# Optimization experiments

Hardware: AMD Instinct MI355X
Metric: run time of the kernel (lower is better)

## Reference

```python
import jax, jax.numpy as jnp
import numpy as np

N_NODES = 50000
N_EDGES = 400000
NUM_FEAT = 11
HID = 64
LAT = 64
HEADS = 3
MAX_NODES = 29
NUM_GRAPHS = 2048
NEG_SLOPE = 0.2


def _w(key, shape):
    return (jax.random.normal(key, shape) * 0.05).astype(jnp.float32)


def setup_inputs() -> dict:
    key = jax.random.key(0)
    ks = jax.random.split(key, 32)
    x = jax.random.normal(ks[0], (N_NODES, NUM_FEAT), dtype=jnp.float32)
    edge_index = jax.random.randint(ks[1], (2, N_EDGES), 0, N_NODES, dtype=jnp.int64)
    batch = jnp.sort(jax.random.randint(ks[2], (N_NODES,), 0, NUM_GRAPHS, dtype=jnp.int64))
    d = {"x": x, "edge_index": edge_index, "batch": batch}
    # GATv2 layer params: lin_l, lin_r ([in, heads*out]), att [heads,out], bias [out]
    dims = [(NUM_FEAT, HID), (HID, 2 * HID), (2 * HID, 4 * HID)]
    k = 3
    for i, (cin, cout) in enumerate(dims, start=1):
        d[f"Wl{i}"] = _w(ks[k], (cin, HEADS * cout)); k += 1
        d[f"bl{i}"] = jnp.zeros((HEADS * cout,), jnp.float32)
        d[f"Wr{i}"] = _w(ks[k], (cin, HEADS * cout)); k += 1
        d[f"br{i}"] = jnp.zeros((HEADS * cout,), jnp.float32)
        d[f"att{i}"] = _w(ks[k], (HEADS, cout)); k += 1
        d[f"b{i}"] = jnp.zeros((cout,), jnp.float32)
    d["Wmu"] = _w(ks[k], (4 * HID, LAT)); k += 1
    d["bmu"] = jnp.zeros((LAT,), jnp.float32)
    d["Wlv"] = _w(ks[k], (4 * HID, LAT)); k += 1
    d["blv"] = jnp.zeros((LAT,), jnp.float32)
    out_dim = MAX_NODES * NUM_FEAT + MAX_NODES * MAX_NODES
    d["Wd1"] = _w(ks[k], (LAT, 4 * HID)); k += 1
    d["bd1"] = jnp.zeros((4 * HID,), jnp.float32)
    d["Wd2"] = _w(ks[k], (4 * HID, 8 * HID)); k += 1
    d["bd2"] = jnp.zeros((8 * HID,), jnp.float32)
    d["Wd3"] = _w(ks[k], (8 * HID, out_dim)); k += 1
    d["bd3"] = jnp.zeros((out_dim,), jnp.float32)
    return d


def _gatv2(x, src, dst, Wl, bl, Wr, br, att, bias):
    # GATv2Conv, heads=HEADS, concat=False (mean over heads), self-loops already in src/dst
    N = x.shape[0]
    H, C = att.shape
    xl = (x @ Wl + bl).reshape(N, H, C)  # source transform
    xr = (x @ Wr + br).reshape(N, H, C)  # target transform
    e = jax.nn.leaky_relu(xl[src] + xr[dst], NEG_SLOPE)  # [E,H,C]
    logits = jnp.einsum('ehc,hc->eh', e, att)            # [E,H]
    mx = jax.ops.segment_max(logits, dst, num_segments=N)
    a = jnp.exp(logits - mx[dst])
    denom = jax.ops.segment_sum(a, dst, num_segments=N)
    alpha = a / (denom[dst] + 1e-16)
    out = jax.ops.segment_sum(alpha[:, :, None] * xl[src], dst, num_segments=N)  # [N,H,C]
    return out.mean(axis=1) + bias


def reference(x, edge_index, batch,
              Wl1, bl1, Wr1, br1, att1, b1,
              Wl2, bl2, Wr2, br2, att2, b2,
              Wl3, bl3, Wr3, br3, att3, b3,
              Wmu, bmu, Wlv, blv,
              Wd1, bd1, Wd2, bd2, Wd3, bd3):
    N = x.shape[0]
    loops = jnp.arange(N, dtype=edge_index.dtype)
    src = jnp.concatenate([edge_index[0], loops])
    dst = jnp.concatenate([edge_index[1], loops])
    h = jax.nn.relu(_gatv2(x, src, dst, Wl1, bl1, Wr1, br1, att1, b1))
    h = jax.nn.relu(_gatv2(h, src, dst, Wl2, bl2, Wr2, br2, att2, b2))
    h = jax.nn.relu(_gatv2(h, src, dst, Wl3, bl3, Wr3, br3, att3, b3))
    g = jax.ops.segment_sum(h, batch, num_segments=NUM_GRAPHS)  # global_add_pool
    mu = g @ Wmu + bmu
    logvar = g @ Wlv + blv
    z = mu  # deterministic decode of the posterior mean (no forward() given)
    o = jax.nn.relu(z @ Wd1 + bd1)
    o = jax.nn.relu(o @ Wd2 + bd2)
    o = o @ Wd3 + bd3
    nsplit = MAX_NODES * NUM_FEAT
    x_rec = o[:, :nsplit].reshape(-1, MAX_NODES, NUM_FEAT)
    adj = o[:, nsplit:].reshape(-1, MAX_NODES, MAX_NODES)
    adj_rec = (adj + jnp.swapaxes(adj, 1, 2)) / 2
    return (x_rec, adj_rec, mu, logvar)
```

## Files before the change

### kernel.cpp

```cpp
#include <hip/hip_runtime.h>
#include <hip/hip_bf16.h>

typedef __hip_bfloat16 bf16;
typedef unsigned short ushortT;
typedef ushortT u16x1 __attribute__((ext_vector_type(1)));
typedef ushortT u16x2 __attribute__((ext_vector_type(2)));
typedef ushortT u16x4 __attribute__((ext_vector_type(4)));
typedef ushortT u16x8 __attribute__((ext_vector_type(8)));
typedef __bf16   bf16x8 __attribute__((ext_vector_type(8)));
typedef float    f32x4  __attribute__((ext_vector_type(4)));

#define N_NODES    50000
#define E_EDGES    400000
#define E_TOT      450000
#define NUM_GRAPHS 2048
#define SCAN_CHUNK 1024
#define N_CHUNKS   ((N_NODES + SCAN_CHUNK - 1) / SCAN_CHUNK)

__device__ __forceinline__ float fromb(ushortT u) {
    unsigned int i = ((unsigned int)u) << 16;
    return __builtin_bit_cast(float, i);
}
__device__ __forceinline__ ushortT tob(float v) {
    bf16 h = __float2bfloat16(v);
    return __builtin_bit_cast(ushortT, h);
}

template <int VEC> struct RawV;
template <> struct RawV<1> { using T = u16x1; };
template <> struct RawV<2> { using T = u16x2; };
template <> struct RawV<4> { using T = u16x4; };

__device__ __forceinline__ void cvtv(u16x1 r, float* f) { f[0] = fromb(r[0]); }
__device__ __forceinline__ void cvtv(u16x2 r, float* f) { f[0] = fromb(r.x); f[1] = fromb(r.y); }
__device__ __forceinline__ void cvtv(u16x4 r, float* f) { f[0] = fromb(r.x); f[1] = fromb(r.y);
                                                          f[2] = fromb(r.z); f[3] = fromb(r.w); }

__global__ void diag_kernel(float* out, float v) { if (threadIdx.x == 0) out[0] = v; }

__global__ void hist_kernel(const int* __restrict__ ei, int* __restrict__ counts) {
    int e = blockIdx.x * 256 + threadIdx.x;
    if (e >= E_TOT) return;
    int d = (e < E_EDGES) ? ei[E_EDGES + e] : (e - E_EDGES);
    atomicAdd(&counts[d], 1);
}

__global__ __launch_bounds__(256) void scan_sums(const int* __restrict__ counts,
                                                 int* __restrict__ chunk_sums) {
    __shared__ int red[4];
    int base = blockIdx.x * SCAN_CHUNK;
    int t = threadIdx.x;
    int s = 0;
    #pragma unroll
    for (int i = 0; i < 4; i++) {
        int idx = base + t + i * 256;
        if (idx < N_NODES) s += counts[idx];
    }
    #pragma unroll
    for (int o = 32; o > 0; o >>= 1) s += __shfl_xor(s, o);
    if ((t & 63) == 0) red[t >> 6] = s;
    __syncthreads();
    if (t == 0) chunk_sums[blockIdx.x] = red[0] + red[1] + red[2] + red[3];
}

__global__ __launch_bounds__(64) void scan_chunks(const int* __restrict__ chunk_sums,
                                                  int* __restrict__ chunk_base) {
    int t = threadIdx.x;
    int v = (t < N_CHUNKS) ? chunk_sums[t] : 0;
    int orig = v;
    #pragma unroll
    for (int o = 1; o < 64; o <<= 1) {
        int u = __shfl_up(v, o);
        if (t >= o) v += u;
    }
    if (t < N_CHUNKS) chunk_base[t] = v - orig;
}

__global__ __launch_bounds__(256) void scan_write(const int* __restrict__ counts,
                                                  const int* __restrict__ chunk_base,
                                                  int* __restrict__ offsets,
                                                  int* __restrict__ cursor) {
    __shared__ int wsum[4];
    int chunk = blockIdx.x;
    int base = chunk * SCAN_CHUNK;
    int t = threadIdx.x;
    int lane = t & 63, w = t >> 6;

    int c[4];
    int e0 = base + t * 4;
    #pragma unroll
    for (int k = 0; k < 4; k++) {
        int idx = e0 + k;
        c[k] = (idx < N_NODES) ? counts[idx] : 0;
    }
    int local = c[0] + c[1] + c[2] + c[3];

    int v = local;
    #pragma unroll
    for (int o = 1; o < 64; o <<= 1) {
        int u = __shfl_up(v, o);
        if (lane >= o) v += u;
    }
    if (lane == 63) wsum[w] = v;
    __syncthreads();
    int wbase = 0;
    for (int i = 0; i < w; i++) wbase += wsum[i];

    int run = chunk_base[chunk] + wbase + (v - local);
    #pragma unroll
    for (int k = 0; k < 4; k++) {
        int idx = e0 + k;
        if (idx < N_NODES) { offsets[idx] = run; cursor[idx] = run; }
        run += c[k];
    }
    if (chunk == 0 && t == 0) offsets[N_NODES] = E_TOT;
}

__global__ void scatter_kernel(const int* __restrict__ ei, int* __restrict__ cursor,
                               int* __restrict__ srcs) {
    int e = blockIdx.x * 256 + threadIdx.x;
    if (e >= E_TOT) return;
    int s, d;
    if (e < E_EDGES) { s = ei[e]; d = ei[E_EDGES + e]; }
    else             { s = d = e - E_EDGES; }
    int pos = atomicAdd(&cursor[d], 1);
    srcs[pos] = s;
}

__global__ void repack_gat_kernel(const float* __restrict__ Wl2, const float* __restrict__ Wr2,
                                  const float* __restrict__ Wl3, const float* __restrict__ Wr3,
                                  ushortT* __restrict__ BpL2, ushortT* __restrict__ BpR2,
                                  ushortT* __restrict__ BpL3, ushortT* __restrict__ BpR3) {
    const int S2 = 64 * 384, S3 = 128 * 768;
    int idx = blockIdx.x * 256 + threadIdx.x;
    const float* W; ushortT* Bp; int N, local;
    if (idx < S2)                { W = Wl2; Bp = BpL2; N = 384; local = idx; }
    else if (idx < 2 * S2)       { W = Wr2; Bp = BpR2; N = 384; local = idx - S2; }
    else if (idx < 2 * S2 + S3)  { W = Wl3; Bp = BpL3; N = 768; local = idx - 2 * S2; }
    else if (idx < 2 * (S2 + S3)){ W = Wr3; Bp = BpR3; N = 768; local = idx - 2 * S2 - S3; }
    else return;
    int k = local / N, n = local % N;
    Bp[((size_t)(k >> 3) * N + n) * 8 + (k & 7)] = tob(W[(size_t)k * N + n]);
}

__global__ void repack_split3(const float* __restrict__ Wd1, const float* __restrict__ Wd2,
                              const float* __restrict__ Wd3,
                              ushortT* __restrict__ BhD1, ushortT* __restrict__ BlD1,
                              ushortT* __restrict__ BhD2, ushortT* __restrict__ BlD2,
                              ushortT* __restrict__ BhD3, ushortT* __restrict__ BlD3) {
    const int T1 = 64 * 256, T2 = 256 * 512, T3 = 512 * 1280;
    int idx = blockIdx.x * 256 + threadIdx.x;
    const float* W; ushortT *Bh, *Bl; int Npad, N, local;
    if (idx < T1)                { W = Wd1; Bh = BhD1; Bl = BlD1; Npad = 256;  N = 256;  local = idx; }
    else if (idx < T1 + T2)      { W = Wd2; Bh = BhD2; Bl = BlD2; Npad = 512;  N = 512;  local = idx - T1; }
    else if (idx < T1 + T2 + T3) { W = Wd3; Bh = BhD3; Bl = BlD3; Npad = 1280; N = 1160; local = idx - T1 - T2; }
    else return;
    int k = local / Npad, n = local % Npad;
    float v = (n < N) ? W[(size_t)k * N + n] : 0.f;
    ushortT h = tob(v);
    size_t o = ((size_t)(k >> 3) * Npad + n) * 8 + (k & 7);
    Bh[o] = h;
    Bl[o] = tob(v - fromb(h));
}

__global__ __launch_bounds__(192) void l1_transform(const float* __restrict__ x,
                                                    const float* __restrict__ Wl,
                                                    const float* __restrict__ bl,
                                                    const float* __restrict__ Wr,
                                                    const float* __restrict__ br,
                                                    ushortT* __restrict__ XL,
                                                    ushortT* __restrict__ XR, int M) {
    __shared__ float xs[64][11];
    const int tid = threadIdx.x;
    const int bm  = blockIdx.x * 64;
    const int rows = (M - bm < 64) ? (M - bm) : 64;

    float wl[11], wr[11];
    #pragma unroll
    for (int k = 0; k < 11; k++) {
        wl[k] = Wl[k * 192 + tid];
        wr[k] = Wr[k * 192 + tid];
    }
    float blc = bl[tid], brc = br[tid];

    for (int i = tid; i < rows * 11; i += 192)
        xs[i / 11][i % 11] = x[(size_t)bm * 11 + i];
    __syncthreads();

    for (int r = 0; r < rows; r++) {
        float al = blc, ar = brc;
        #pragma unroll
        for (int k = 0; k < 11; k++) {
            float xv = xs[r][k];
            al += xv * wl[k];
            ar += xv * wr[k];
        }
        size_t o = (size_t)(bm + r) * 192 + tid;
        XL[o] = tob(al);
        XR[o] = tob(ar);
    }
}

template <bool RELU>
__global__ __launch_bounds__(256) void gemm_dec(const float* __restrict__ A,
                                                const float* __restrict__ B,
                                                const float* __restrict__ bias,
                                                float* __restrict__ C,
                                                int M, int N, int K,
                                                int lda, int ldb, int ldc) {
    __shared__ float As[32][33];
    __shared__ float Bs[32][65];
    int tid = threadIdx.x;
    int tm = tid >> 4, tn = tid & 15;
    int bm = blockIdx.y * 32, bn = blockIdx.x * 64;
    float acc[2][4] = {};
    for (int k0 = 0; k0 < K; k0 += 32) {
        #pragma unroll
        for (int i = 0; i < 4; i++) {
            int e = tid + i * 256;
            int r = e >> 5, k = e & 31;
            int row = bm + r, kk = k0 + k;
            float v = 0.f;
            if (row < M && kk < K) v = A[(size_t)row * lda + kk];
            As[k][r] = v;
        }
        #pragma unroll
        for (int i = 0; i < 8; i++) {
            int e = tid + i * 256;
            int k = e >> 6, n = e & 63;
            int kk = k0 + k, col = bn + n;
            float v = 0.f;
            if (kk < K && col < N) v = B[(size_t)kk * ldb + col];
            Bs[k][n] = v;
        }
        __syncthreads();
        #pragma unroll
        for (int k = 0; k < 32; k++) {
            float a0 = As[k][tm * 2 + 0], a1 = As[k][tm * 2 + 1];
            float b0 = Bs[k][tn * 4 + 0], b1 = Bs[k][tn * 4 + 1];
            float b2 = Bs[k][tn * 4 + 2], b3 = Bs[k][tn * 4 + 3];
            acc[0][0] += a0 * b0; acc[0][1] += a0 * b1; acc[0][2] += a0 * b2; acc[0][3] += a0 * b3;
            acc[1][0] += a1 * b0; acc[1][1] += a1 * b1; acc[1][2] += a1 * b2; acc[1][3] += a1 * b3;
        }
        __syncthreads();
    }
    #pragma unroll
    for (int i = 0; i < 2; i++) {
        int row = bm + tm * 2 + i;
        if (row >= M) continue;
        #pragma unroll
        for (int j = 0; j < 4; j++) {
            int col = bn + tn * 4 + j;
            if (col >= N) continue;
            float v = acc[i][j] + bias[col];
            if (RELU) v = fmaxf(v, 0.f);
            C[(size_t)row * ldc + col] = v;
        }
    }
}

template <bool RELU>
__global__ __launch_bounds__(256) void mfma_dec(const float* __restrict__ A,
                                                const ushortT* __restrict__ Bh,
                                                const ushortT* __restrict__ Bl,
                                                const float* __restrict__ bias,
                                                float* __restrict__ C,
                                                int M, int N, int K, int Npad,
                                                int lda, int ldc) {
    __shared__ ushortT Ah[4 * 128 * 8];
    __shared__ ushortT Al[4 * 128 * 8];
    const int tid = threadIdx.x;
    const int bm = blockIdx.y * 128;
    const int bn = blockIdx.x * 128;
    const int lane = tid & 63;
    const int l15 = lane & 15, lg = lane >> 4;
    const int wid = tid >> 6;
    const int wm = wid >> 1, wn = wid & 1;

    f32x4 acc[4][4] = {};

    for (int k0 = 0; k0 < K; k0 += 32) {
        __syncthreads();
        #pragma unroll
        for (int it = 0; it < 2; it++) {
            int c = tid + it * 256;
            int row = c >> 2, kg = c & 3;
            const float* ap = A + (size_t)(bm + row) * lda + k0 + kg * 8;
            u16x8 hv, lv;
            #pragma unroll
            for (int i = 0; i < 8; i++) {
                float v = ap[i];
                ushortT h = tob(v);
                hv[i] = h;
                lv[i] = tob(v - fromb(h));
            }
            int unit = (kg * 128 + row) ^ kg;
            *reinterpret_cast<u16x8*>(&Ah[unit * 8]) = hv;
            *reinterpret_cast<u16x8*>(&Al[unit * 8]) = lv;
        }
        __syncthreads();

        bf16x8 ah[4], al[4], bhf[4], blf[4];
        #pragma unroll
        for (int mf = 0; mf < 4; mf++) {
            int row = wm * 64 + mf * 16 + l15;
            int unit = (lg * 128 + row) ^ lg;
            ah[mf] = __builtin_bit_cast(bf16x8, *reinterpret_cast<const u16x8*>(&Ah[unit * 8]));
            al[mf] = __builtin_bit_cast(bf16x8, *reinterpret_cast<const u16x8*>(&Al[unit * 8]));
        }
        int kgG = (k0 >> 3) + lg;
        #pragma unroll
        for (int nf = 0; nf < 4; nf++) {
            int n = bn + wn * 64 + nf * 16 + l15;
            size_t o = ((size_t)kgG * Npad + n) * 8;
            bhf[nf] = __builtin_bit_cast(bf16x8, *reinterpret_cast<const u16x8*>(Bh + o));
            blf[nf] = __builtin_bit_cast(bf16x8, *reinterpret_cast<const u16x8*>(Bl + o));
        }
        #pragma unroll
        for (int mf = 0; mf < 4; mf++) {
            #pragma unroll
            for (int nf = 0; nf < 4; nf++) {
                acc[mf][nf] = __builtin_amdgcn_mfma_f32_16x16x32_bf16(ah[mf], bhf[nf], acc[mf][nf], 0, 0, 0);
                acc[mf][nf] = __builtin_amdgcn_mfma_f32_16x16x32_bf16(ah[mf], blf[nf], acc[mf][nf], 0, 0, 0);
                acc[mf][nf] = __builtin_amdgcn_mfma_f32_16x16x32_bf16(al[mf], bhf[nf], acc[mf][nf], 0, 0, 0);
            }
        }
    }

    #pragma unroll
    for (int nf = 0; nf < 4; nf++) {
        int col = bn + wn * 64 + nf * 16 + l15;
        if (col >= N) continue;
        float bv = bias[col];
        #pragma unroll
        for (int mf = 0; mf < 4; mf++) {
            #pragma unroll
            for (int q = 0; q < 4; q++) {
                int row = bm + wm * 64 + mf * 16 + lg * 4 + q;
                if (row < M) {
                    float v = acc[mf][nf][q] + bv;
                    if (RELU) v = fmaxf(v, 0.f);
                    C[(size_t)row * ldc + col] = v;
                }
            }
        }
    }
}

template <int K, int NW>
__global__ __launch_bounds__(256) void mfma_gemmF(const ushortT* __restrict__ A,
                                                  const ushortT* __restrict__ BpL,
                                                  const ushortT* __restrict__ BpR,
                                                  const float* __restrict__ bl,
                                                  const float* __restrict__ br,
                                                  bf16* __restrict__ XL,
                                                  bf16* __restrict__ XR,
                                                  int M) {
    constexpr int KU = K / 8;
    __shared__ ushortT Alds[KU * 128 * 8];
    const int tid = threadIdx.x;
    const int bm  = blockIdx.y * 128;
    const int bnb = blockIdx.x * 128;

    for (int u = tid; u < 128 * KU; u += 256) {
        int row = u / KU, kg = u % KU;
        int rg = bm + row; if (rg > M - 1) rg = M - 1;
        u16x8 v = *reinterpret_cast<const u16x8*>(A + (size_t)rg * K + kg * 8);
        int unit = (kg * 128 + row) ^ (kg & 7);
        *reinterpret_cast<u16x8*>(&Alds[unit * 8]) = v;
    }
    __syncthreads();

    const int lane = tid & 63;
    const int l15 = lane & 15, lg = lane >> 4;
    const int wid = tid >> 6;
    const int wm = wid >> 1, wn = wid & 1;

    f32x4 acc[4][4] = {};
    #pragma unroll
    for (int s = 0; s < K / 32; s++) {
        int kg = s * 4 + lg;
        bf16x8 a[4], b[4];
        #pragma unroll
        for (int mf = 0; mf < 4; mf++) {
            int row = wm * 64 + mf * 16 + l15;
            int unit = (kg * 128 + row) ^ (kg & 7);
            a[mf] = __builtin_bit_cast(bf16x8,
                    *reinterpret_cast<const u16x8*>(&Alds[unit * 8]));
        }
        #pragma unroll
        for (int nf = 0; nf < 4; nf++) {
            int cb = bnb + wn * 64 + nf * 16;
            const ushortT* bp; int n;
            if (cb < NW) { bp = BpL; n = cb + l15; }
            else         { bp = BpR; n = cb - NW + l15; }
            b[nf] = __builtin_bit_cast(bf16x8,
                    *reinterpret_cast<const u16x8*>(bp + ((size_t)kg * NW + n) * 8));
        }
        #pragma unroll
        for (int mf = 0; mf < 4; mf++)
            #pragma unroll
            for (int nf = 0; nf < 4; nf++)
                acc[mf][nf] = __builtin_amdgcn_mfma_f32_16x16x32_bf16(
                    a[mf], b[nf], acc[mf][nf], 0, 0, 0);
    }

    #pragma unroll
    for (int nf = 0; nf < 4; nf++) {
        int cb = bnb + wn * 64 + nf * 16;
        bf16* Cp; const float* bs; int c;
        if (cb < NW) { Cp = XL; bs = bl; c = cb + l15; }
        else         { Cp = XR; bs = br; c = cb - NW + l15; }
        float bv = bs[c];
        #pragma unroll
        for (int mf = 0; mf < 4; mf++) {
            #pragma unroll
            for (int q = 0; q < 4; q++) {
                int r = bm + wm * 64 + mf * 16 + lg * 4 + q;
                if (r < M) Cp[(size_t)r * NW + c] = __float2bfloat16(acc[mf][nf][q] + bv);
            }
        }
    }
}

template <int CHH>
__global__ __launch_bounds__(256) void gat_fused(const ushortT* __restrict__ XL,
                                                 const ushortT* __restrict__ XR,
                                                 const float* __restrict__ att,
                                                 const float* __restrict__ bias,
                                                 const int* __restrict__ offsets,
                                                 const int* __restrict__ srcs,
                                                 ushortT* __restrict__ OUT, int N) {
    constexpr int VEC = CHH / 64;
    constexpr int LDX = 3 * CHH;
    using RT = typename RawV<VEC>::T;
    int wid  = threadIdx.x >> 6;
    int lane = threadIdx.x & 63;
    int n = blockIdx.x * 4 + wid;
    if (n >= N) return;

    const int loff = VEC * lane;
    float xr_[3][VEC], a06[3][VEC], a04[3][VEC], acc[3][VEC];
    const ushortT* xrp = XR + (size_t)n * LDX + loff;
    #pragma unroll
    for (int h = 0; h < 3; h++) {
        RT xrv = *reinterpret_cast<const RT*>(xrp + h * CHH);
        #pragma unroll
        for (int i = 0; i < VEC; i++) {
            xr_[h][i] = fromb(xrv[i]);
            float a = att[h * CHH + loff + i];
            a06[h][i] = 0.6f * a;
            a04[h][i] = 0.4f * a;
            acc[h][i] = 0.f;
        }
    }
    float d0 = 0.f, d1 = 0.f, d2 = 0.f;

    const int e0 = offsets[n];
    const int deg = offsets[n + 1] - e0;

    for (int base = 0; base < deg; base += 64) {
        int cnt = deg - base; if (cnt > 64) cnt = 64;
        int sl = srcs[e0 + base + ((lane < cnt) ? lane : (cnt - 1))];

        RT A0, A1, A2, B0, B1, B2, C0, C1, C2;
        {
            const ushortT* r = XL + (size_t)__shfl(sl, 0) * LDX + loff;
            A0 = *reinterpret_cast<const RT*>(r);
            A1 = *reinterpret_cast<const RT*>(r + CHH);
            A2 = *reinterpret_cast<const RT*>(r + 2 * CHH);
        }
        if (cnt > 1) {
            const ushortT* r = XL + (size_t)__shfl(sl, 1) * LDX + loff;
            B0 = *reinterpret_cast<const RT*>(r);
            B1 = *reinterpret_cast<const RT*>(r + CHH);
            B2 = *reinterpret_cast<const RT*>(r + 2 * CHH);
        } else { B0 = A0; B1 = A1; B2 = A2; }
        if (cnt > 2) {
            const ushortT* r = XL + (size_t)__shfl(sl, 2) * LDX + loff;
            C0 = *reinterpret_cast<const RT*>(r);
            C1 = *reinterpret_cast<const RT*>(r + CHH);
            C2 = *reinterpret_cast<const RT*>(r + 2 * CHH);
        } else { C0 = A0; C1 = A1; C2 = A2; }

        for (int j = 0; j < cnt; ++j) {
            RT c0 = A0, c1 = A1, c2 = A2;
            A0 = B0; A1 = B1; A2 = B2;
            B0 = C0; B1 = C1; B2 = C2;
            if (j + 3 < cnt) {
                const ushortT* r = XL + (size_t)__shfl(sl, j + 3) * LDX + loff;
                C0 = *reinterpret_cast<const RT*>(r);
                C1 = *reinterpret_cast<const RT*>(r + CHH);
                C2 = *reinterpret_cast<const RT*>(r + 2 * CHH);
            }

            float xl0[VEC], xl1[VEC], xl2[VEC];
            cvtv(c0, xl0); cvtv(c1, xl1); cvtv(c2, xl2);
            float p0 = 0.f, p1 = 0.f, p2 = 0.f;
            #pragma unroll
            for (int i = 0; i < VEC; i++) {
                float v0 = xl0[i] + xr_[0][i];
                float v1 = xl1[i] + xr_[1][i];
                float v2 = xl2[i] + xr_[2][i];
                p0 = fmaf(a06[0][i], v0, p0); p0 = fmaf(a04[0][i], fabsf(v0), p0);
                p1 = fmaf(a06[1][i], v1, p1); p1 = fmaf(a04[1][i], fabsf(v1), p1);
                p2 = fmaf(a06[2][i], v2, p2); p2 = fmaf(a04[2][i], fabsf(v2), p2);
            }
            #pragma unroll
            for (int ofs = 32; ofs > 0; ofs >>= 1) {
                p0 += __shfl_xor(p0, ofs);
                p1 += __shfl_xor(p1, ofs);
                p2 += __shfl_xor(p2, ofs);
            }

            float w0 = __expf(p0), w1 = __expf(p1), w2 = __expf(p2);
            d0 += w0; d1 += w1; d2 += w2;
            #pragma unroll
            for (int i = 0; i < VEC; i++) {
                acc[0][i] = fmaf(w0, xl0[i], acc[0][i]);
                acc[1][i] = fmaf(w1, xl1[i], acc[1][i]);
                acc[2][i] = fmaf(w2, xl2[i], acc[2][i]);
            }
        }
    }

    float i0 = 1.f / (d0 + 1e-16f);
    float i1 = 1.f / (d1 + 1e-16f);
    float i2 = 1.f / (d2 + 1e-16f);
    RT ov;
    #pragma unroll
    for (int i = 0; i < VEC; i++) {
        int c = loff + i;
        float v = (acc[0][i] * i0 + acc[1][i] * i1 + acc[2][i] * i2) * (1.f / 3.f) + bias[c];
        ov[i] = tob(fmaxf(v, 0.f));
    }
    *reinterpret_cast<RT*>(&OUT[(size_t)n * CHH + loff]) = ov;
}

__global__ void pool_kernel(const ushortT* __restrict__ h3, const int* __restrict__ batch,
                            float* __restrict__ G) {
    int g = blockIdx.x;
    int c = threadIdx.x;
    int lo = 0, hi = N_NODES;
    while (lo < hi) { int mid = (lo + hi) >> 1; if (batch[mid] < g) lo = mid + 1; else hi = mid; }
    int s0 = lo;
    hi = N_NODES;
    while (lo < hi) { int mid = (lo + hi) >> 1; if (batch[mid] < g + 1) lo = mid + 1; else hi = mid; }
    int s1 = lo;
    float sum = 0.f;
    for (int n = s0; n < s1; n++) sum += fromb(h3[(size_t)n * 256 + c]);
    G[(size_t)g * 256 + c] = sum;
}

__global__ void assemble_kernel(const float* __restrict__ o3, float* __restrict__ out) {
    int g = blockIdx.x;
    const float* row = o3 + (size_t)g * 1160;
    float* xrec = out + (size_t)g * 319;
    for (int p = threadIdx.x; p < 319; p += 256) xrec[p] = row[p];
    float* adj = out + 653312 + (size_t)g * 841;
    for (int p = threadIdx.x; p < 841; p += 256) {
        int i = p / 29, j = p % 29;
        adj[p] = 0.5f * (row[319 + p] + row[319 + j * 29 + i]);
    }
}

extern "C" void kernel_launch(void* const* d_in, const int* in_sizes, int n_in,
                              void* d_out, int out_size, void* d_ws, size_t ws_size,
                              hipStream_t stream) {
    const float* x     = (const float*)d_in[0];
    const int*   ei    = (const int*)d_in[1];
    const int*   batch = (const int*)d_in[2];
    const float* Wl1 = (const float*)d_in[3];
    const float* bl1 = (const float*)d_in[4];
    const float* Wr1 = (const float*)d_in[5];
    const float* br1 = (const float*)d_in[6];
    const float* att1= (const float*)d_in[7];
    const float* b1  = (const float*)d_in[8];
    const float* Wl2 = (const float*)d_in[9];
    const float* bl2 = (const float*)d_in[10];
    const float* Wr2 = (const float*)d_in[11];
    const float* br2 = (const float*)d_in[12];
    const float* att2= (const float*)d_in[13];
    const float* b2  = (const float*)d_in[14];
    const float* Wl3 = (const float*)d_in[15];
    const float* bl3 = (const float*)d_in[16];
    const float* Wr3 = (const float*)d_in[17];
    const float* br3 = (const float*)d_in[18];
    const float* att3= (const float*)d_in[19];
    const float* b3  = (const float*)d_in[20];
    const float* Wmu = (const float*)d_in[21];
    const float* bmu = (const float*)d_in[22];
    const float* Wlv = (const float*)d_in[23];
    const float* blv = (const float*)d_in[24];
    const float* Wd1 = (const float*)d_in[25];
    const float* bd1 = (const float*)d_in[26];
    const float* Wd2 = (const float*)d_in[27];
    const float* bd2 = (const float*)d_in[28];
    const float* Wd3 = (const float*)d_in[29];
    const float* bd3 = (const float*)d_in[30];
    float* out = (float*)d_out;

    const int MU_OFF = 2375680;
    const int LV_OFF = 2506752;
    char* wsb = (char*)d_ws;

    const size_t NEED_FULL = 194892064;
    const dim3 AGG_GRID(N_NODES / 4);

    if (ws_size < NEED_FULL) {
        hipLaunchKernelGGL(diag_kernel, dim3(1), dim3(64), 0, stream, out, (float)(ws_size >> 20));
        return;
    }

    ushortT* h3u = (ushortT*)(wsb + 0);
    ushortT* h1u = (ushortT*)(wsb + 0);
    ushortT* h2u = (ushortT*)(wsb + 25600000);
    bf16*    XLb = (bf16*)(wsb + 38400000);
    ushortT* XLu = (ushortT*)(wsb + 38400000);
    bf16*    XRb = (bf16*)(wsb + 115200000);
    ushortT* XRu = (ushortT*)(wsb + 115200000);
    float* G  = (float*)(wsb + 38400000);
    float* O1 = G  + 524288;
    float* O2 = O1 + 524288;
    float* O3 = O2 + 1048576;
    ushortT* BhD3 = (ushortT*)(wsb + 115200000);
    ushortT* BlD3 = (ushortT*)(wsb + 116600000);
    ushortT* BhD2 = (ushortT*)(wsb + 118000000);
    ushortT* BlD2 = (ushortT*)(wsb + 118300000);
    ushortT* BhD1 = (ushortT*)(wsb + 118600000);
    ushortT* BlD1 = (ushortT*)(wsb + 118700000);
    int* counts  = (int*)(wsb + 192000000);
    int* offsets = counts + (N_NODES + 1);
    int* cursor  = offsets + (N_NODES + 1);
    int* srcs    = cursor + (N_NODES + 1);
    int* chunk_sums = srcs + E_TOT;
    int* chunk_base = chunk_sums + 64;
    ushortT* BpL2 = (ushortT*)(wsb + 194400544);
    ushortT* BpR2 = (ushortT*)(wsb + 194449696);
    ushortT* BpL3 = (ushortT*)(wsb + 194498848);
    ushortT* BpR3 = (ushortT*)(wsb + 194695456);

    hipMemsetAsync(counts, 0, sizeof(int) * (N_NODES + 1), stream);
    hipLaunchKernelGGL(hist_kernel, dim3((E_TOT + 255) / 256), dim3(256), 0, stream, ei, counts);
    hipLaunchKernelGGL(scan_sums,   dim3(N_CHUNKS), dim3(256), 0, stream, counts, chunk_sums);
    hipLaunchKernelGGL(scan_chunks, dim3(1), dim3(64), 0, stream, chunk_sums, chunk_base);
    hipLaunchKernelGGL(scan_write,  dim3(N_CHUNKS), dim3(256), 0, stream,
                       counts, chunk_base, offsets, cursor);
    hipLaunchKernelGGL(scatter_kernel, dim3((E_TOT + 255) / 256), dim3(256), 0, stream,
                       ei, cursor, srcs);

    hipLaunchKernelGGL(repack_gat_kernel, dim3(960), dim3(256), 0, stream,
                       Wl2, Wr2, Wl3, Wr3, BpL2, BpR2, BpL3, BpR3);

    hipLaunchKernelGGL(l1_transform, dim3((N_NODES + 63) / 64), dim3(192), 0, stream,
                       x, Wl1, bl1, Wr1, br1, XLu, XRu, N_NODES);
    hipLaunchKernelGGL((gat_fused<64>), AGG_GRID, dim3(256), 0, stream,
                       XLu, XRu, att1, b1, offsets, srcs, h1u, N_NODES);
    hipLaunchKernelGGL((mfma_gemmF<64, 384>), dim3(6, 391), dim3(256), 0, stream,
                       h1u, BpL2, BpR2, bl2, br2, XLb, XRb, N_NODES);
    hipLaunchKernelGGL((gat_fused<128>), AGG_GRID, dim3(256), 0, stream,
                       XLu, XRu, att2, b2, offsets, srcs, h2u, N_NODES);
    hipLaunchKernelGGL((mfma_gemmF<128, 768>), dim3(12, 391), dim3(256), 0, stream,
                       h2u, BpL3, BpR3, bl3, br3, XLb, XRb, N_NODES);
    hipLaunchKernelGGL((gat_fused<256>), AGG_GRID, dim3(256), 0, stream,
                       XLu, XRu, att3, b3, offsets, srcs, h3u, N_NODES);

    hipLaunchKernelGGL(repack_split3, dim3(3136), dim3(256), 0, stream,
                       Wd1, Wd2, Wd3, BhD1, BlD1, BhD2, BlD2, BhD3, BlD3);

    hipLaunchKernelGGL(pool_kernel, dim3(NUM_GRAPHS), dim3(256), 0, stream, h3u, batch, G);

    hipLaunchKernelGGL((gemm_dec<false>), dim3(1, 64), dim3(256), 0, stream,
                       G, Wmu, bmu, out + MU_OFF, NUM_GRAPHS, 64, 256, 256, 64, 64);
    hipLaunchKernelGGL((gemm_dec<false>), dim3(1, 64), dim3(256), 0, stream,
                       G, Wlv, blv, out + LV_OFF, NUM_GRAPHS, 64, 256, 256, 64, 64);
    hipLaunchKernelGGL((mfma_dec<true>), dim3(2, 16), dim3(256), 0, stream,
                       out + MU_OFF, BhD1, BlD1, bd1, O1, NUM_GRAPHS, 256, 64, 256, 64, 256);
    hipLaunchKernelGGL((mfma_dec<true>), dim3(4, 16), dim3(256), 0, stream,
                       O1, BhD2, BlD2, bd2, O2, NUM_GRAPHS, 512, 256, 512, 256, 512);
    hipLaunchKernelGGL((mfma_dec<false>), dim3(10, 16), dim3(256), 0, stream,
                       O2, BhD3, BlD3, bd3, O3, NUM_GRAPHS, 1160, 512, 1280, 512, 1160);
    hipLaunchKernelGGL(assemble_kernel, dim3(NUM_GRAPHS), dim3(256), 0, stream, O3, out);
}
```

Baseline: 833.5 us.

## Make GAT aggregation persistent with grid-stride nodes and shallower 2-deep prefetch

The GATv2 aggregation kernel becomes persistent: a fixed grid of 2048 blocks grid-strides over nodes, so attention and bias loads are hoisted out of the per-node work. The 3-deep register prefetch of source rows is replaced by a 2-deep ping-pong buffer, which lowers register pressure. The divide by three is folded into the softmax normalisation. The intent is to cut launch and wave-setup overhead and raise occupancy, at the cost of less memory-latency hiding per wave and possible load imbalance across waves.

```diff
diff --git a/kernel.cpp b/kernel.cpp
--- a/kernel.cpp
+++ b/kernel.cpp
@@ -434,66 +434,39 @@
     constexpr int VEC = CHH / 64;
     constexpr int LDX = 3 * CHH;
     using RT = typename RawV<VEC>::T;
-    int wid  = threadIdx.x >> 6;
-    int lane = threadIdx.x & 63;
-    int n = blockIdx.x * 4 + wid;
-    if (n >= N) return;
-
+    const int lane = threadIdx.x & 63;
+    const int wave = blockIdx.x * 4 + (threadIdx.x >> 6);
+    const int WTOT = gridDim.x * 4;
     const int loff = VEC * lane;
-    float xr_[3][VEC], a06[3][VEC], a04[3][VEC], acc[3][VEC];
-    const ushortT* xrp = XR + (size_t)n * LDX + loff;
+
+    float a06[3][VEC], a04[3][VEC], bi[VEC];
     #pragma unroll
     for (int h = 0; h < 3; h++) {
-        RT xrv = *reinterpret_cast<const RT*>(xrp + h * CHH);
         #pragma unroll
         for (int i = 0; i < VEC; i++) {
-            xr_[h][i] = fromb(xrv[i]);
             float a = att[h * CHH + loff + i];
             a06[h][i] = 0.6f * a;
             a04[h][i] = 0.4f * a;
-            acc[h][i] = 0.f;
-        }
-    }
-    float d0 = 0.f, d1 = 0.f, d2 = 0.f;
-
-    const int e0 = offsets[n];
-    const int deg = offsets[n + 1] - e0;
-
-    for (int base = 0; base < deg; base += 64) {
-        int cnt = deg - base; if (cnt > 64) cnt = 64;
-        int sl = srcs[e0 + base + ((lane < cnt) ? lane : (cnt - 1))];
-
-        RT A0, A1, A2, B0, B1, B2, C0, C1, C2;
-        {
-            const ushortT* r = XL + (size_t)__shfl(sl, 0) * LDX + loff;
-            A0 = *reinterpret_cast<const RT*>(r);
-            A1 = *reinterpret_cast<const RT*>(r + CHH);
-            A2 = *reinterpret_cast<const RT*>(r + 2 * CHH);
-        }
-        if (cnt > 1) {
-            const ushortT* r = XL + (size_t)__shfl(sl, 1) * LDX + loff;
-            B0 = *reinterpret_cast<const RT*>(r);
-            B1 = *reinterpret_cast<const RT*>(r + CHH);
-            B2 = *reinterpret_cast<const RT*>(r + 2 * CHH);
-        } else { B0 = A0; B1 = A1; B2 = A2; }
-        if (cnt > 2) {
-            const ushortT* r = XL + (size_t)__shfl(sl, 2) * LDX + loff;
-            C0 = *reinterpret_cast<const RT*>(r);
-            C1 = *reinterpret_cast<const RT*>(r + CHH);
-            C2 = *reinterpret_cast<const RT*>(r + 2 * CHH);
-        } else { C0 = A0; C1 = A1; C2 = A2; }
-
-        for (int j = 0; j < cnt; ++j) {
-            RT c0 = A0, c1 = A1, c2 = A2;
-            A0 = B0; A1 = B1; A2 = B2;
-            B0 = C0; B1 = C1; B2 = C2;
-            if (j + 3 < cnt) {
-                const ushortT* r = XL + (size_t)__shfl(sl, j + 3) * LDX + loff;
-                C0 = *reinterpret_cast<const RT*>(r);
-                C1 = *reinterpret_cast<const RT*>(r + CHH);
-                C2 = *reinterpret_cast<const RT*>(r + 2 * CHH);
-            }
-
+        }
+    }
+    #pragma unroll
+    for (int i = 0; i < VEC; i++) bi[i] = bias[loff + i];
+
+    for (int n = wave; n < N; n += WTOT) {
+        float xr_[3][VEC], acc[3][VEC];
+        const ushortT* xrp = XR + (size_t)n * LDX + loff;
+        #pragma unroll
+        for (int h = 0; h < 3; h++) {
+            RT xrv = *reinterpret_cast<const RT*>(xrp + h * CHH);
+            #pragma unroll
+            for (int i = 0; i < VEC; i++) { xr_[h][i] = fromb(xrv[i]); acc[h][i] = 0.f; }
+        }
+        float d0 = 0.f, d1 = 0.f, d2 = 0.f;
+
+        const int e0 = offsets[n];
+        const int deg = offsets[n + 1] - e0;
+
+        auto process = [&](RT c0, RT c1, RT c2) {
             float xl0[VEC], xl1[VEC], xl2[VEC];
             cvtv(c0, xl0); cvtv(c1, xl1); cvtv(c2, xl2);
             float p0 = 0.f, p1 = 0.f, p2 = 0.f;
@@ -512,7 +485,6 @@
                 p1 += __shfl_xor(p1, ofs);
                 p2 += __shfl_xor(p2, ofs);
             }
-
             float w0 = __expf(p0), w1 = __expf(p1), w2 = __expf(p2);
             d0 += w0; d1 += w1; d2 += w2;
             #pragma unroll
@@ -521,20 +493,50 @@
                 acc[1][i] = fmaf(w1, xl1[i], acc[1][i]);
                 acc[2][i] = fmaf(w2, xl2[i], acc[2][i]);
             }
-        }
-    }
-
-    float i0 = 1.f / (d0 + 1e-16f);
-    float i1 = 1.f / (d1 + 1e-16f);
-    float i2 = 1.f / (d2 + 1e-16f);
-    RT ov;
-    #pragma unroll
-    for (int i = 0; i < VEC; i++) {
-        int c = loff + i;
-        float v = (acc[0][i] * i0 + acc[1][i] * i1 + acc[2][i] * i2) * (1.f / 3.f) + bias[c];
-        ov[i] = tob(fmaxf(v, 0.f));
-    }
-    *reinterpret_cast<RT*>(&OUT[(size_t)n * CHH + loff]) = ov;
+        };
+
+        for (int base = 0; base < deg; base += 64) {
+            int cnt = deg - base; if (cnt > 64) cnt = 64;
+            int sl = srcs[e0 + base + ((lane < cnt) ? lane : (cnt - 1))];
+
+            RT A0, A1, A2, B0, B1, B2;
+            {
+                const ushortT* r = XL + (size_t)__shfl(sl, 0) * LDX + loff;
+                A0 = *reinterpret_cast<const RT*>(r);
+                A1 = *reinterpret_cast<const RT*>(r + CHH);
+                A2 = *reinterpret_cast<const RT*>(r + 2 * CHH);
+            }
+            for (int j = 0; j < cnt; j += 2) {
+                if (j + 1 < cnt) {
+                    const ushortT* r = XL + (size_t)__shfl(sl, j + 1) * LDX + loff;
+                    B0 = *reinterpret_cast<const RT*>(r);
+                    B1 = *reinterpret_cast<const RT*>(r + CHH);
+                    B2 = *reinterpret_cast<const RT*>(r + 2 * CHH);
+                }
+                process(A0, A1, A2);
+                if (j + 1 < cnt) {
+                    if (j + 2 < cnt) {
+                        const ushortT* r = XL + (size_t)__shfl(sl, j + 2) * LDX + loff;
+                        A0 = *reinterpret_cast<const RT*>(r);
+                        A1 = *reinterpret_cast<const RT*>(r + CHH);
+                        A2 = *reinterpret_cast<const RT*>(r + 2 * CHH);
+                    }
+                    process(B0, B1, B2);
+                }
+            }
+        }
+
+        float i0 = 1.f / (3.f * d0 + 1e-16f);
+        float i1 = 1.f / (3.f * d1 + 1e-16f);
+        float i2 = 1.f / (3.f * d2 + 1e-16f);
+        RT ov;
+        #pragma unroll
+        for (int i = 0; i < VEC; i++) {
+            float v = acc[0][i] * i0 + acc[1][i] * i1 + acc[2][i] * i2 + bi[i];
+            ov[i] = tob(fmaxf(v, 0.f));
+        }
+        *reinterpret_cast<RT*>(&OUT[(size_t)n * CHH + loff]) = ov;
+    }
 }
 
 __global__ void pool_kernel(const ushortT* __restrict__ h3, const int* __restrict__ batch,
@@ -605,7 +607,7 @@
     char* wsb = (char*)d_ws;
 
     const size_t NEED_FULL = 194892064;
-    const dim3 AGG_GRID(N_NODES / 4);
+    const dim3 AGG_GRID(2048);
 
     if (ws_size < NEED_FULL) {
         hipLaunchKernelGGL(diag_kernel, dim3(1), dim3(64), 0, stream, out, (float)(ws_size >> 20));
```

Result: slower. 862.4 us (+3.5%).
